# Performance work log

Hardware: AMD Instinct MI355X
Metric: run time of the kernel (lower is better)

Reference implementation:

```python
import jax, jax.numpy as jnp
import numpy as np

HIDDEN = 4096
MOE_INTER = 1024
SHARED_INTER = 4096  # intermediate_size * num_shared_expert
NUM_EXPERTS = 16
TOP_K = 2


def setup_inputs() -> dict:
    key = jax.random.key(0)
    ks = jax.random.split(key, 6)
    s = 0.02
    hidden_states = jax.random.normal(ks[0], (2, 2048, HIDDEN), dtype=jnp.float32)
    gate_w = jax.random.normal(ks[1], (NUM_EXPERTS, HIDDEN), dtype=jnp.float32) * s
    # per-expert SwiGLU weights: gate_up [E, 2I, H], down [E, H, I]
    w_gate_up = jax.random.normal(ks[2], (NUM_EXPERTS, 2 * MOE_INTER, HIDDEN), dtype=jnp.float32) * s
    w_down = jax.random.normal(ks[3], (NUM_EXPERTS, HIDDEN, MOE_INTER), dtype=jnp.float32) * s
    shared_w_gate_up = jax.random.normal(ks[4], (2 * SHARED_INTER, HIDDEN), dtype=jnp.float32) * s
    shared_w_down = jax.random.normal(ks[5], (HIDDEN, SHARED_INTER), dtype=jnp.float32) * s
    return {
        'hidden_states': hidden_states,
        'gate_w': gate_w,
        'w_gate_up': w_gate_up,
        'w_down': w_down,
        'shared_w_gate_up': shared_w_gate_up,
        'shared_w_down': shared_w_down,
    }


def _moe_forward(x, gate_w, w_gate_up, w_down, shared_w_gate_up, shared_w_down):
    orig_shape = x.shape
    x2 = x.reshape(-1, orig_shape[-1])  # [T, H]

    # shared SwiGLU MLP (reduce_results=False in TP; single device here)
    gu_s = x2 @ shared_w_gate_up.T  # [T, 2*Is]
    g_s, u_s = jnp.split(gu_s, 2, axis=-1)
    shared_out = (jax.nn.silu(g_s) * u_s) @ shared_w_down.T  # [T, H]

    # router: softmax -> top-k -> renormalize (top_k > 1)
    logits = x2 @ gate_w.T  # [T, E]
    probs = jax.nn.softmax(logits, axis=-1)
    topk_vals, topk_idx = jax.lax.top_k(probs, TOP_K)  # [T, K]
    topk_vals = topk_vals / jnp.sum(topk_vals, axis=-1, keepdims=True)
    # combine weights [T, E]: sparse top-k weights scattered into dense matrix
    combine = jnp.sum(
        jax.nn.one_hot(topk_idx, NUM_EXPERTS, dtype=x2.dtype) * topk_vals[..., None],
        axis=1,
    )

    # dense per-expert SwiGLU (reference for fused grouped-GEMM)
    gu = jnp.einsum('th,eih->eti', x2, w_gate_up)  # [E, T, 2I]
    g, u = jnp.split(gu, 2, axis=-1)
    act = jax.nn.silu(g) * u  # [E, T, I]
    out_e = jnp.einsum('eti,ehi->eth', act, w_down)  # [E, T, H]
    moe_out = jnp.einsum('eth,te->th', out_e, combine)  # [T, H]

    return (moe_out + shared_out).reshape(orig_shape)


def reference(hidden_states, gate_w, w_gate_up, w_down, shared_w_gate_up, shared_w_down):
    return _moe_forward(hidden_states, gate_w, w_gate_up, w_down,
                        shared_w_gate_up, shared_w_down)
```

## Files before the change

### kernel.cpp

```cpp
#include <hip/hip_runtime.h>
#include <hip/hip_bf16.h>

#define H 4096
#define MOE_I 1024
#define SH_I 4096
#define NE 16
#define T_TOK 4096
#define NPAIR 8192

using bf16x8 = __attribute__((ext_vector_type(8))) short;
using f32x4  = __attribute__((ext_vector_type(4))) float;

__device__ __forceinline__ unsigned short f2bf(float f) {
    unsigned int x = __float_as_uint(f);
    x += 0x7fffu + ((x >> 16) & 1u);
    return (unsigned short)(x >> 16);
}
__device__ __forceinline__ float bf2f(unsigned short u) {
    return __uint_as_float(((unsigned int)u) << 16);
}

__device__ __forceinline__ void gld_lds16(const void* g, void* l) {
    __builtin_amdgcn_global_load_lds(
        (const __attribute__((address_space(1))) void*)g,
        (__attribute__((address_space(3))) void*)l, 16, 0, 0);
}

__global__ __launch_bounds__(256)
void cast_kernel(const float4* __restrict__ src, ushort4* __restrict__ dst, int n4) {
    int i = blockIdx.x * 256 + threadIdx.x;
    if (i < n4) {
        float4 f = src[i];
        ushort4 o;
        o.x = f2bf(f.x); o.y = f2bf(f.y); o.z = f2bf(f.z); o.w = f2bf(f.w);
        dst[i] = o;
    }
}

__global__ __launch_bounds__(256)
void router_kernel(const float* __restrict__ x, const float* __restrict__ gw,
                   int* __restrict__ topk_id, float* __restrict__ topk_w,
                   int* __restrict__ counts) {
    int t = blockIdx.x;
    const float* xr = x + (size_t)t * H;
    __shared__ float lg[NE];
    int tid = threadIdx.x, w = tid >> 6, lane = tid & 63;
#pragma unroll
    for (int i = 0; i < 4; i++) {
        int e = w * 4 + i;
        const float* g = gw + (size_t)e * H;
        float s = 0.f;
        for (int k = lane; k < H; k += 64) s += xr[k] * g[k];
#pragma unroll
        for (int m = 32; m > 0; m >>= 1) s += __shfl_xor(s, m, 64);
        if (lane == 0) lg[e] = s;
    }
    __syncthreads();
    if (tid == 0) {
        int e0 = 0; float l0 = lg[0];
        for (int e = 1; e < NE; e++) if (lg[e] > l0) { l0 = lg[e]; e0 = e; }
        int e1 = -1; float l1 = -1e30f;
        for (int e = 0; e < NE; e++) if (e != e0 && lg[e] > l1) { l1 = lg[e]; e1 = e; }
        float w1 = 1.f / (1.f + __expf(l0 - l1));
        topk_id[2*t] = e0; topk_id[2*t+1] = e1;
        topk_w[2*t] = 1.f - w1; topk_w[2*t+1] = w1;
        atomicAdd(&counts[e0], 1); atomicAdd(&counts[e1], 1);
    }
}

__global__ void scan16(const int* __restrict__ counts, int* __restrict__ offsets,
                       int* __restrict__ cursor) {
    if (threadIdx.x == 0 && blockIdx.x == 0) {
        int s = 0;
        for (int e = 0; e < NE; e++) { offsets[e] = s; cursor[e] = s; s += counts[e]; }
        offsets[NE] = s;
    }
}

__global__ __launch_bounds__(256)
void assign_kernel(const int* __restrict__ topk_id, const float* __restrict__ topk_w,
                   int* __restrict__ cursor, int* __restrict__ perm_tok,
                   float* __restrict__ perm_w) {
    int t = blockIdx.x * blockDim.x + threadIdx.x;
    if (t >= T_TOK) return;
    for (int k = 0; k < 2; k++) {
        int e = topk_id[2*t+k];
        int pos = atomicAdd(&cursor[e], 1);
        perm_tok[pos] = t;
        perm_w[pos] = topk_w[2*t+k];
    }
}

template<int MODE>
__global__ __launch_bounds__(512, 2)
void gemm8(const unsigned short* __restrict__ A0,
           const unsigned short* __restrict__ B0,
           unsigned short* __restrict__ Cb, float* __restrict__ Cf,
           const int* __restrict__ offsets, const int* __restrict__ perm_tok,
           const float* __restrict__ perm_w,
           int K, int N, int M, int ldc) {
    extern __shared__ char smem[];
    int e = 0, off = 0, cnt = M;
    if constexpr (MODE >= 2) { e = blockIdx.z; off = offsets[e]; cnt = offsets[e + 1] - off; }
    const int m0 = blockIdx.y * 256, n0 = blockIdx.x * 256;
    if (m0 >= cnt) return;
    const unsigned short* Bp = B0 + (size_t)e * N * K;

    const int tid = threadIdx.x, w = tid >> 6, lane = tid & 63;
    const int wr = w >> 2, wc = w & 3;
    const int quad = lane >> 4, r16 = lane & 15;

    const unsigned short* srcA[2][2];
    const unsigned short* srcB[2][2];
    int dstA[2][2], dstB[2][2];
#pragma unroll
    for (int kh = 0; kh < 2; kh++)
#pragma unroll
        for (int j = 0; j < 2; j++) {
            int D  = (j * 8 + w) * 1024 + lane * 16;
            int r  = D >> 6;
            int sl = (D >> 4) & 3;
            int sg = sl ^ ((r >> 1) & 3);
            int ra = m0 + r; if (ra > cnt - 1) ra = cnt - 1;
            int rs;
            if constexpr (MODE == 2)      rs = perm_tok[off + ra];
            else if constexpr (MODE == 3) rs = off + ra;
            else                          rs = ra;
            srcA[kh][j] = A0 + (size_t)rs * K + kh * 32 + sg * 8;
            srcB[kh][j] = Bp + (size_t)(n0 + r) * K + kh * 32 + sg * 8;
            dstA[kh][j] = kh * 16384 + (j * 8 + w) * 1024;
            dstB[kh][j] = 32768 + dstA[kh][j];
        }

    const int swz  = (quad ^ ((r16 >> 1) & 3)) * 16;
    const int aoff = (wr * 128 + r16) * 64 + swz;
    const int boff = 32768 + (wc * 64 + r16) * 64 + swz;

    f32x4 acc[8][4];
#pragma unroll
    for (int i = 0; i < 8; i++)
#pragma unroll
        for (int j = 0; j < 4; j++) acc[i][j] = (f32x4){0.f, 0.f, 0.f, 0.f};

    const int nt = K >> 6;

#pragma unroll
    for (int kh = 0; kh < 2; kh++) {
        gld_lds16(srcA[kh][0], smem + dstA[kh][0]);
        gld_lds16(srcA[kh][1], smem + dstA[kh][1]);
        gld_lds16(srcB[kh][0], smem + dstB[kh][0]);
        gld_lds16(srcB[kh][1], smem + dstB[kh][1]);
    }
    {
        int adv0 = (nt > 1) ? 64 : 0;
#pragma unroll
        for (int kh = 0; kh < 2; kh++)
#pragma unroll
            for (int j = 0; j < 2; j++) { srcA[kh][j] += adv0; srcB[kh][j] += adv0; }
    }

    for (int t = 0; t < nt; t++) {
        char* sb = smem + (t & 1) * 65536;
        char* so = smem + ((t + 1) & 1) * 65536;
        const int adv = (t + 2 < nt) ? 64 : 0;
        bf16x8 av[4], bv[4];

        asm volatile("s_waitcnt vmcnt(4)" ::: "memory");
        __builtin_amdgcn_s_barrier();
        asm volatile("" ::: "memory");
        gld_lds16(srcA[0][0], so + dstA[0][0]);
        gld_lds16(srcA[0][1], so + dstA[0][1]);
        srcA[0][0] += adv; srcA[0][1] += adv;
#pragma unroll
        for (int mi = 0; mi < 4; mi++) av[mi] = *(const bf16x8*)(sb + mi * 1024 + aoff);
#pragma unroll
        for (int ni = 0; ni < 4; ni++) bv[ni] = *(const bf16x8*)(sb + ni * 1024 + boff);
        __builtin_amdgcn_s_setprio(1);
#pragma unroll
        for (int mi = 0; mi < 4; mi++)
#pragma unroll
            for (int ni = 0; ni < 4; ni++)
                acc[mi][ni] = __builtin_amdgcn_mfma_f32_16x16x32_bf16(
                    av[mi], bv[ni], acc[mi][ni], 0, 0, 0);
        __builtin_amdgcn_s_setprio(0);
        gld_lds16(srcB[0][0], so + dstB[0][0]);
        gld_lds16(srcB[0][1], so + dstB[0][1]);
        srcB[0][0] += adv; srcB[0][1] += adv;
#pragma unroll
        for (int mi = 0; mi < 4; mi++) av[mi] = *(const bf16x8*)(sb + (mi + 4) * 1024 + aoff);
        __builtin_amdgcn_s_setprio(1);
#pragma unroll
        for (int mi = 0; mi < 4; mi++)
#pragma unroll
            for (int ni = 0; ni < 4; ni++)
                acc[mi + 4][ni] = __builtin_amdgcn_mfma_f32_16x16x32_bf16(
                    av[mi], bv[ni], acc[mi + 4][ni], 0, 0, 0);
        __builtin_amdgcn_s_setprio(0);

        asm volatile("s_waitcnt vmcnt(4)" ::: "memory");
        __builtin_amdgcn_s_barrier();
        asm volatile("" ::: "memory");
        gld_lds16(srcA[1][0], so + dstA[1][0]);
        gld_lds16(srcA[1][1], so + dstA[1][1]);
        srcA[1][0] += adv; srcA[1][1] += adv;
#pragma unroll
        for (int mi = 0; mi < 4; mi++) av[mi] = *(const bf16x8*)(sb + 16384 + mi * 1024 + aoff);
#pragma unroll
        for (int ni = 0; ni < 4; ni++) bv[ni] = *(const bf16x8*)(sb + 16384 + ni * 1024 + boff);
        __builtin_amdgcn_s_setprio(1);
#pragma unroll
        for (int mi = 0; mi < 4; mi++)
#pragma unroll
            for (int ni = 0; ni < 4; ni++)
                acc[mi][ni] = __builtin_amdgcn_mfma_f32_16x16x32_bf16(
                    av[mi], bv[ni], acc[mi][ni], 0, 0, 0);
        __builtin_amdgcn_s_setprio(0);
        gld_lds16(srcB[1][0], so + dstB[1][0]);
        gld_lds16(srcB[1][1], so + dstB[1][1]);
        srcB[1][0] += adv; srcB[1][1] += adv;
#pragma unroll
        for (int mi = 0; mi < 4; mi++) av[mi] = *(const bf16x8*)(sb + 16384 + (mi + 4) * 1024 + aoff);
        __builtin_amdgcn_s_setprio(1);
#pragma unroll
        for (int mi = 0; mi < 4; mi++)
#pragma unroll
            for (int ni = 0; ni < 4; ni++)
                acc[mi + 4][ni] = __builtin_amdgcn_mfma_f32_16x16x32_bf16(
                    av[mi], bv[ni], acc[mi + 4][ni], 0, 0, 0);
        __builtin_amdgcn_s_setprio(0);
    }

    asm volatile("s_waitcnt vmcnt(0)" ::: "memory");

    const int rowlim = cnt - m0;
#pragma unroll
    for (int mi = 0; mi < 8; mi++) {
#pragma unroll
        for (int rr = 0; rr < 4; rr++) {
            int r = wr * 128 + mi * 16 + quad * 4 + rr;
            if (r < rowlim) {
                int tok = 0; float wt = 0.f;
                if constexpr (MODE == 3) {
                    tok = perm_tok[off + m0 + r];
                    wt  = perm_w[off + m0 + r];
                }
#pragma unroll
                for (int ni = 0; ni < 4; ni++) {
                    int col = n0 + wc * 64 + ni * 16 + r16;
                    float v = acc[mi][ni][rr];
                    if constexpr (MODE == 0)
                        Cb[(size_t)(m0 + r) * ldc + col] = f2bf(v);
                    else if constexpr (MODE == 1)
                        Cf[(size_t)(m0 + r) * ldc + col] = v;
                    else if constexpr (MODE == 2)
                        Cb[(size_t)(off + m0 + r) * ldc + col] = f2bf(v);
                    else
                        atomicAdd(&Cf[(size_t)tok * ldc + col], wt * v);
                }
            }
        }
    }
}

template<int SHIFT>
__global__ __launch_bounds__(256)
void swiglu_kernel(const unsigned short* __restrict__ gu, unsigned short* __restrict__ act,
                   long long total) {
    long long idx = ((long long)blockIdx.x * 256 + threadIdx.x) * 8;
    if (idx >= total) return;
    const int half = 1 << SHIFT;
    long long row = idx >> SHIFT;
    int cb = (int)(idx & (half - 1));
    const unsigned short* gp = gu + (row << (SHIFT + 1)) + cb;
    bf16x8 g8 = *(const bf16x8*)gp;
    bf16x8 u8 = *(const bf16x8*)(gp + half);
    bf16x8 res;
#pragma unroll
    for (int i = 0; i < 8; i++) {
        float g = bf2f((unsigned short)g8[i]);
        float u = bf2f((unsigned short)u8[i]);
        float a = g / (1.f + __expf(-g));
        res[i] = (short)f2bf(a * u);
    }
    *(bf16x8*)(act + idx) = res;
}

extern "C" void kernel_launch(void* const* d_in, const int* in_sizes, int n_in,
                              void* d_out, int out_size, void* d_ws, size_t ws_size,
                              hipStream_t stream) {
    const float* x         = (const float*)d_in[0];
    const float* gate_w    = (const float*)d_in[1];
    const float* w_gate_up = (const float*)d_in[2];
    const float* w_down    = (const float*)d_in[3];
    const float* s_wgu     = (const float*)d_in[4];
    const float* s_wd      = (const float*)d_in[5];
    float* out = (float*)d_out;

    char* p = (char*)d_ws;
    auto alloc = [&](size_t bytes) {
        char* q = p;
        p += (bytes + 255) & ~(size_t)255;
        return q;
    };
    unsigned short* x_bf    = (unsigned short*)alloc((size_t)T_TOK * H * 2);
    unsigned short* wgu_bf  = (unsigned short*)alloc((size_t)NE * 2 * MOE_I * H * 2);
    unsigned short* wd_bf   = (unsigned short*)alloc((size_t)NE * H * MOE_I * 2);
    unsigned short* swgu_bf = (unsigned short*)alloc((size_t)2 * SH_I * H * 2);
    unsigned short* swd_bf  = (unsigned short*)alloc((size_t)H * SH_I * 2);
    unsigned short* gu_s    = (unsigned short*)alloc((size_t)T_TOK * 2 * SH_I * 2);
    unsigned short* act_s   = (unsigned short*)alloc((size_t)T_TOK * SH_I * 2);
    unsigned short* gu_e    = (unsigned short*)alloc((size_t)NPAIR * 2 * MOE_I * 2);
    unsigned short* act_e   = (unsigned short*)alloc((size_t)NPAIR * MOE_I * 2);
    int*   topk_id  = (int*)alloc(T_TOK * 2 * 4);
    float* topk_w   = (float*)alloc(T_TOK * 2 * 4);
    int*   counts   = (int*)alloc(NE * 4);
    int*   offsets  = (int*)alloc((NE + 1) * 4);
    int*   cursor   = (int*)alloc(NE * 4);
    int*   perm_tok = (int*)alloc(NPAIR * 4);
    float* perm_w   = (float*)alloc(NPAIR * 4);

    hipMemsetAsync(counts, 0, 768, stream);

    const int SHMEM = 131072;
    static int attr_done = 0;
    if (!attr_done) {
        hipFuncSetAttribute((const void*)gemm8<0>, hipFuncAttributeMaxDynamicSharedMemorySize, SHMEM);
        hipFuncSetAttribute((const void*)gemm8<1>, hipFuncAttributeMaxDynamicSharedMemorySize, SHMEM);
        hipFuncSetAttribute((const void*)gemm8<2>, hipFuncAttributeMaxDynamicSharedMemorySize, SHMEM);
        hipFuncSetAttribute((const void*)gemm8<3>, hipFuncAttributeMaxDynamicSharedMemorySize, SHMEM);
        attr_done = 1;
    }

    auto cast = [&](const float* s, unsigned short* d, size_t n) {
        int n4 = (int)(n / 4);
        cast_kernel<<<(n4 + 255) / 256, 256, 0, stream>>>((const float4*)s, (ushort4*)d, n4);
    };
    cast(x, x_bf, (size_t)T_TOK * H);
    cast(w_gate_up, wgu_bf, (size_t)NE * 2 * MOE_I * H);
    cast(w_down, wd_bf, (size_t)NE * H * MOE_I);
    cast(s_wgu, swgu_bf, (size_t)2 * SH_I * H);
    cast(s_wd, swd_bf, (size_t)H * SH_I);

    router_kernel<<<T_TOK, 256, 0, stream>>>(x, gate_w, topk_id, topk_w, counts);
    scan16<<<1, 64, 0, stream>>>(counts, offsets, cursor);
    assign_kernel<<<16, 256, 0, stream>>>(topk_id, topk_w, cursor, perm_tok, perm_w);

    gemm8<0><<<dim3(2 * SH_I / 256, T_TOK / 256, 1), 512, SHMEM, stream>>>(
        x_bf, swgu_bf, gu_s, nullptr, nullptr, nullptr, nullptr, H, 2 * SH_I, T_TOK, 2 * SH_I);
    swiglu_kernel<12><<<(int)(((long long)T_TOK * SH_I / 8 + 255) / 256), 256, 0, stream>>>(
        gu_s, act_s, (long long)T_TOK * SH_I);
    gemm8<1><<<dim3(H / 256, T_TOK / 256, 1), 512, SHMEM, stream>>>(
        act_s, swd_bf, nullptr, out, nullptr, nullptr, nullptr, SH_I, H, T_TOK, H);

    gemm8<2><<<dim3(2 * MOE_I / 256, T_TOK / 256, NE), 512, SHMEM, stream>>>(
        x_bf, wgu_bf, gu_e, nullptr, offsets, perm_tok, nullptr, H, 2 * MOE_I, 0, 2 * MOE_I);
    swiglu_kernel<10><<<(int)(((long long)NPAIR * MOE_I / 8 + 255) / 256), 256, 0, stream>>>(
        gu_e, act_e, (long long)NPAIR * MOE_I);
    gemm8<3><<<dim3(H / 256, T_TOK / 256, NE), 512, SHMEM, stream>>>(
        act_e, wd_bf, nullptr, out, offsets, perm_tok, perm_w, MOE_I, H, 0, H);
}
```

Measured before the change: 2.073 ms.

## Fuse weight bf16 casting into GEMM B-loads and SwiGLU into gate-up epilogue

The separate fp32-to-bf16 cast kernels for all weight matrices are removed. Each GEMM now reads fp32 weights through registers, converts them with packed bf16 conversion and writes them into swizzled LDS, software-pipelined across the k loop. The gate-up GEMMs interleave gate and up rows so that neighbouring columns pair up, and they apply SiLU*up in the epilogue, which removes the standalone swiglu kernels and the intermediate gate-up buffers. The cost is twice the weight bytes fetched per tile and register-staged loads in place of direct global-to-LDS loads, which may hurt the main-loop throughput.

```diff
diff --git a/kernel.cpp b/kernel.cpp
--- a/kernel.cpp
+++ b/kernel.cpp
@@ -18,6 +18,11 @@
 }
 __device__ __forceinline__ float bf2f(unsigned short u) {
     return __uint_as_float(((unsigned int)u) << 16);
+}
+__device__ __forceinline__ unsigned int cvtpk(float lo, float hi) {
+    unsigned int r;
+    asm("v_cvt_pk_bf16_f32 %0, %1, %2" : "=v"(r) : "v"(lo), "v"(hi));
+    return r;
 }
 
 __device__ __forceinline__ void gld_lds16(const void* g, void* l) {
@@ -94,7 +99,7 @@
 template<int MODE>
 __global__ __launch_bounds__(512, 2)
 void gemm8(const unsigned short* __restrict__ A0,
-           const unsigned short* __restrict__ B0,
+           const float* __restrict__ B0f,
            unsigned short* __restrict__ Cb, float* __restrict__ Cf,
            const int* __restrict__ offsets, const int* __restrict__ perm_tok,
            const float* __restrict__ perm_w,
@@ -104,15 +109,14 @@
     if constexpr (MODE >= 2) { e = blockIdx.z; off = offsets[e]; cnt = offsets[e + 1] - off; }
     const int m0 = blockIdx.y * 256, n0 = blockIdx.x * 256;
     if (m0 >= cnt) return;
-    const unsigned short* Bp = B0 + (size_t)e * N * K;
+    const float* Bp = B0f + (size_t)e * N * K;
 
     const int tid = threadIdx.x, w = tid >> 6, lane = tid & 63;
     const int wr = w >> 2, wc = w & 3;
     const int quad = lane >> 4, r16 = lane & 15;
 
     const unsigned short* srcA[2][2];
-    const unsigned short* srcB[2][2];
-    int dstA[2][2], dstB[2][2];
+    int dstA[2][2];
 #pragma unroll
     for (int kh = 0; kh < 2; kh++)
 #pragma unroll
@@ -127,10 +131,24 @@
             else if constexpr (MODE == 3) rs = off + ra;
             else                          rs = ra;
             srcA[kh][j] = A0 + (size_t)rs * K + kh * 32 + sg * 8;
-            srcB[kh][j] = Bp + (size_t)(n0 + r) * K + kh * 32 + sg * 8;
             dstA[kh][j] = kh * 16384 + (j * 8 + w) * 1024;
-            dstB[kh][j] = 32768 + dstA[kh][j];
-        }
+        }
+
+    const int r_t  = tid >> 4;
+    const int kcol = (tid & 15) * 4;
+    const float* bsrc;
+    size_t rstride;
+    if constexpr (MODE == 0 || MODE == 2) {
+        int n = n0 + r_t;
+        int sr = (n >> 1) + (n & 1) * (N >> 1);
+        bsrc = Bp + (size_t)sr * K + kcol;
+        rstride = (size_t)16 * K;
+    } else {
+        bsrc = Bp + (size_t)(n0 + r_t) * K + kcol;
+        rstride = (size_t)32 * K;
+    }
+    const int bw0 = 32768 + (kcol >> 5) * 16384 + r_t * 64
+                  + ((((kcol & 31) >> 3) ^ ((r_t >> 1) & 3)) * 16) + (kcol & 7) * 2;
 
     const int swz  = (quad ^ ((r16 >> 1) & 3)) * 16;
     const int aoff = (wr * 128 + r16) * 64 + swz;
@@ -144,33 +162,41 @@
 
     const int nt = K >> 6;
 
-#pragma unroll
-    for (int kh = 0; kh < 2; kh++) {
-        gld_lds16(srcA[kh][0], smem + dstA[kh][0]);
-        gld_lds16(srcA[kh][1], smem + dstA[kh][1]);
-        gld_lds16(srcB[kh][0], smem + dstB[kh][0]);
-        gld_lds16(srcB[kh][1], smem + dstB[kh][1]);
+    gld_lds16(srcA[0][0], smem + dstA[0][0]);
+    gld_lds16(srcA[0][1], smem + dstA[0][1]);
+    {
+        float4 b0[8];
+#pragma unroll
+        for (int i = 0; i < 8; i++) b0[i] = *(const float4*)(bsrc + (size_t)i * rstride);
+        gld_lds16(srcA[1][0], smem + dstA[1][0]);
+        gld_lds16(srcA[1][1], smem + dstA[1][1]);
+#pragma unroll
+        for (int i = 0; i < 8; i++) {
+            uint2 u2; u2.x = cvtpk(b0[i].x, b0[i].y); u2.y = cvtpk(b0[i].z, b0[i].w);
+            *(uint2*)(smem + bw0 + i * 2048) = u2;
+        }
     }
     {
         int adv0 = (nt > 1) ? 64 : 0;
 #pragma unroll
         for (int kh = 0; kh < 2; kh++)
 #pragma unroll
-            for (int j = 0; j < 2; j++) { srcA[kh][j] += adv0; srcB[kh][j] += adv0; }
+            for (int j = 0; j < 2; j++) srcA[kh][j] += adv0;
+        bsrc += adv0;
     }
 
     for (int t = 0; t < nt; t++) {
         char* sb = smem + (t & 1) * 65536;
         char* so = smem + ((t + 1) & 1) * 65536;
-        const int adv = (t + 2 < nt) ? 64 : 0;
+        const int advA = (t + 2 < nt) ? 64 : 0;
         bf16x8 av[4], bv[4];
-
-        asm volatile("s_waitcnt vmcnt(4)" ::: "memory");
+        float4 bld[8];
+
+        asm volatile("s_waitcnt lgkmcnt(0)" ::: "memory");
         __builtin_amdgcn_s_barrier();
-        asm volatile("" ::: "memory");
         gld_lds16(srcA[0][0], so + dstA[0][0]);
         gld_lds16(srcA[0][1], so + dstA[0][1]);
-        srcA[0][0] += adv; srcA[0][1] += adv;
+        srcA[0][0] += advA; srcA[0][1] += advA;
 #pragma unroll
         for (int mi = 0; mi < 4; mi++) av[mi] = *(const bf16x8*)(sb + mi * 1024 + aoff);
 #pragma unroll
@@ -183,9 +209,10 @@
                 acc[mi][ni] = __builtin_amdgcn_mfma_f32_16x16x32_bf16(
                     av[mi], bv[ni], acc[mi][ni], 0, 0, 0);
         __builtin_amdgcn_s_setprio(0);
-        gld_lds16(srcB[0][0], so + dstB[0][0]);
-        gld_lds16(srcB[0][1], so + dstB[0][1]);
-        srcB[0][0] += adv; srcB[0][1] += adv;
+        __builtin_amdgcn_sched_barrier(0);
+#pragma unroll
+        for (int i = 0; i < 8; i++) bld[i] = *(const float4*)(bsrc + (size_t)i * rstride);
+        __builtin_amdgcn_sched_barrier(0);
 #pragma unroll
         for (int mi = 0; mi < 4; mi++) av[mi] = *(const bf16x8*)(sb + (mi + 4) * 1024 + aoff);
         __builtin_amdgcn_s_setprio(1);
@@ -197,12 +224,11 @@
                     av[mi], bv[ni], acc[mi + 4][ni], 0, 0, 0);
         __builtin_amdgcn_s_setprio(0);
 
-        asm volatile("s_waitcnt vmcnt(4)" ::: "memory");
+        asm volatile("s_waitcnt vmcnt(10)" ::: "memory");
         __builtin_amdgcn_s_barrier();
-        asm volatile("" ::: "memory");
         gld_lds16(srcA[1][0], so + dstA[1][0]);
         gld_lds16(srcA[1][1], so + dstA[1][1]);
-        srcA[1][0] += adv; srcA[1][1] += adv;
+        srcA[1][0] += advA; srcA[1][1] += advA;
 #pragma unroll
         for (int mi = 0; mi < 4; mi++) av[mi] = *(const bf16x8*)(sb + 16384 + mi * 1024 + aoff);
 #pragma unroll
@@ -215,9 +241,12 @@
                 acc[mi][ni] = __builtin_amdgcn_mfma_f32_16x16x32_bf16(
                     av[mi], bv[ni], acc[mi][ni], 0, 0, 0);
         __builtin_amdgcn_s_setprio(0);
-        gld_lds16(srcB[1][0], so + dstB[1][0]);
-        gld_lds16(srcB[1][1], so + dstB[1][1]);
-        srcB[1][0] += adv; srcB[1][1] += adv;
+#pragma unroll
+        for (int i = 0; i < 8; i++) {
+            uint2 u2; u2.x = cvtpk(bld[i].x, bld[i].y); u2.y = cvtpk(bld[i].z, bld[i].w);
+            *(uint2*)(so + bw0 + i * 2048) = u2;
+        }
+        bsrc += (t + 2 < nt) ? 64 : 0;
 #pragma unroll
         for (int mi = 0; mi < 4; mi++) av[mi] = *(const bf16x8*)(sb + 16384 + (mi + 4) * 1024 + aoff);
         __builtin_amdgcn_s_setprio(1);
@@ -233,56 +262,50 @@
     asm volatile("s_waitcnt vmcnt(0)" ::: "memory");
 
     const int rowlim = cnt - m0;
-#pragma unroll
-    for (int mi = 0; mi < 8; mi++) {
-#pragma unroll
-        for (int rr = 0; rr < 4; rr++) {
-            int r = wr * 128 + mi * 16 + quad * 4 + rr;
-            if (r < rowlim) {
-                int tok = 0; float wt = 0.f;
-                if constexpr (MODE == 3) {
-                    tok = perm_tok[off + m0 + r];
-                    wt  = perm_w[off + m0 + r];
-                }
+    if constexpr (MODE == 0 || MODE == 2) {
+#pragma unroll
+        for (int mi = 0; mi < 8; mi++) {
+#pragma unroll
+            for (int rr = 0; rr < 4; rr++) {
+                int r = wr * 128 + mi * 16 + quad * 4 + rr;
 #pragma unroll
                 for (int ni = 0; ni < 4; ni++) {
-                    int col = n0 + wc * 64 + ni * 16 + r16;
-                    float v = acc[mi][ni][rr];
-                    if constexpr (MODE == 0)
-                        Cb[(size_t)(m0 + r) * ldc + col] = f2bf(v);
-                    else if constexpr (MODE == 1)
-                        Cf[(size_t)(m0 + r) * ldc + col] = v;
-                    else if constexpr (MODE == 2)
-                        Cb[(size_t)(off + m0 + r) * ldc + col] = f2bf(v);
-                    else
-                        atomicAdd(&Cf[(size_t)tok * ldc + col], wt * v);
+                    float g = acc[mi][ni][rr];
+                    float u = __shfl_xor(g, 1, 64);
+                    if (((r16 & 1) == 0) && (r < rowlim)) {
+                        float a = (g / (1.f + __expf(-g))) * u;
+                        size_t row = (MODE == 0) ? (size_t)(m0 + r) : (size_t)(off + m0 + r);
+                        int colh = (n0 >> 1) + wc * 32 + ni * 8 + (r16 >> 1);
+                        Cb[row * ldc + colh] = f2bf(a);
+                    }
                 }
             }
         }
-    }
-}
-
-template<int SHIFT>
-__global__ __launch_bounds__(256)
-void swiglu_kernel(const unsigned short* __restrict__ gu, unsigned short* __restrict__ act,
-                   long long total) {
-    long long idx = ((long long)blockIdx.x * 256 + threadIdx.x) * 8;
-    if (idx >= total) return;
-    const int half = 1 << SHIFT;
-    long long row = idx >> SHIFT;
-    int cb = (int)(idx & (half - 1));
-    const unsigned short* gp = gu + (row << (SHIFT + 1)) + cb;
-    bf16x8 g8 = *(const bf16x8*)gp;
-    bf16x8 u8 = *(const bf16x8*)(gp + half);
-    bf16x8 res;
-#pragma unroll
-    for (int i = 0; i < 8; i++) {
-        float g = bf2f((unsigned short)g8[i]);
-        float u = bf2f((unsigned short)u8[i]);
-        float a = g / (1.f + __expf(-g));
-        res[i] = (short)f2bf(a * u);
-    }
-    *(bf16x8*)(act + idx) = res;
+    } else {
+#pragma unroll
+        for (int mi = 0; mi < 8; mi++) {
+#pragma unroll
+            for (int rr = 0; rr < 4; rr++) {
+                int r = wr * 128 + mi * 16 + quad * 4 + rr;
+                if (r < rowlim) {
+                    int tok = 0; float wt = 0.f;
+                    if constexpr (MODE == 3) {
+                        tok = perm_tok[off + m0 + r];
+                        wt  = perm_w[off + m0 + r];
+                    }
+#pragma unroll
+                    for (int ni = 0; ni < 4; ni++) {
+                        int col = n0 + wc * 64 + ni * 16 + r16;
+                        float v = acc[mi][ni][rr];
+                        if constexpr (MODE == 1)
+                            Cf[(size_t)(m0 + r) * ldc + col] = v;
+                        else
+                            atomicAdd(&Cf[(size_t)tok * ldc + col], wt * v);
+                    }
+                }
+            }
+        }
+    }
 }
 
 extern "C" void kernel_launch(void* const* d_in, const int* in_sizes, int n_in,
@@ -302,15 +325,9 @@
         p += (bytes + 255) & ~(size_t)255;
         return q;
     };
-    unsigned short* x_bf    = (unsigned short*)alloc((size_t)T_TOK * H * 2);
-    unsigned short* wgu_bf  = (unsigned short*)alloc((size_t)NE * 2 * MOE_I * H * 2);
-    unsigned short* wd_bf   = (unsigned short*)alloc((size_t)NE * H * MOE_I * 2);
-    unsigned short* swgu_bf = (unsigned short*)alloc((size_t)2 * SH_I * H * 2);
-    unsigned short* swd_bf  = (unsigned short*)alloc((size_t)H * SH_I * 2);
-    unsigned short* gu_s    = (unsigned short*)alloc((size_t)T_TOK * 2 * SH_I * 2);
-    unsigned short* act_s   = (unsigned short*)alloc((size_t)T_TOK * SH_I * 2);
-    unsigned short* gu_e    = (unsigned short*)alloc((size_t)NPAIR * 2 * MOE_I * 2);
-    unsigned short* act_e   = (unsigned short*)alloc((size_t)NPAIR * MOE_I * 2);
+    unsigned short* x_bf   = (unsigned short*)alloc((size_t)T_TOK * H * 2);
+    unsigned short* act_s  = (unsigned short*)alloc((size_t)T_TOK * SH_I * 2);
+    unsigned short* act_e  = (unsigned short*)alloc((size_t)NPAIR * MOE_I * 2);
     int*   topk_id  = (int*)alloc(T_TOK * 2 * 4);
     float* topk_w   = (float*)alloc(T_TOK * 2 * 4);
     int*   counts   = (int*)alloc(NE * 4);
@@ -331,31 +348,22 @@
         attr_done = 1;
     }
 
-    auto cast = [&](const float* s, unsigned short* d, size_t n) {
-        int n4 = (int)(n / 4);
-        cast_kernel<<<(n4 + 255) / 256, 256, 0, stream>>>((const float4*)s, (ushort4*)d, n4);
-    };
-    cast(x, x_bf, (size_t)T_TOK * H);
-    cast(w_gate_up, wgu_bf, (size_t)NE * 2 * MOE_I * H);
-    cast(w_down, wd_bf, (size_t)NE * H * MOE_I);
-    cast(s_wgu, swgu_bf, (size_t)2 * SH_I * H);
-    cast(s_wd, swd_bf, (size_t)H * SH_I);
+    {
+        int n4 = (int)((size_t)T_TOK * H / 4);
+        cast_kernel<<<(n4 + 255) / 256, 256, 0, stream>>>((const float4*)x, (ushort4*)x_bf, n4);
+    }
 
     router_kernel<<<T_TOK, 256, 0, stream>>>(x, gate_w, topk_id, topk_w, counts);
     scan16<<<1, 64, 0, stream>>>(counts, offsets, cursor);
     assign_kernel<<<16, 256, 0, stream>>>(topk_id, topk_w, cursor, perm_tok, perm_w);
 
     gemm8<0><<<dim3(2 * SH_I / 256, T_TOK / 256, 1), 512, SHMEM, stream>>>(
-        x_bf, swgu_bf, gu_s, nullptr, nullptr, nullptr, nullptr, H, 2 * SH_I, T_TOK, 2 * SH_I);
-    swiglu_kernel<12><<<(int)(((long long)T_TOK * SH_I / 8 + 255) / 256), 256, 0, stream>>>(
-        gu_s, act_s, (long long)T_TOK * SH_I);
+        x_bf, s_wgu, act_s, nullptr, nullptr, nullptr, nullptr, H, 2 * SH_I, T_TOK, SH_I);
     gemm8<1><<<dim3(H / 256, T_TOK / 256, 1), 512, SHMEM, stream>>>(
-        act_s, swd_bf, nullptr, out, nullptr, nullptr, nullptr, SH_I, H, T_TOK, H);
+        act_s, s_wd, nullptr, out, nullptr, nullptr, nullptr, SH_I, H, T_TOK, H);
 
     gemm8<2><<<dim3(2 * MOE_I / 256, T_TOK / 256, NE), 512, SHMEM, stream>>>(
-        x_bf, wgu_bf, gu_e, nullptr, offsets, perm_tok, nullptr, H, 2 * MOE_I, 0, 2 * MOE_I);
-    swiglu_kernel<10><<<(int)(((long long)NPAIR * MOE_I / 8 + 255) / 256), 256, 0, stream>>>(
-        gu_e, act_e, (long long)NPAIR * MOE_I);
+        x_bf, w_gate_up, act_e, nullptr, offsets, perm_tok, nullptr, H, 2 * MOE_I, 0, MOE_I);
     gemm8<3><<<dim3(H / 256, T_TOK / 256, NE), 512, SHMEM, stream>>>(
-        act_e, wd_bf, nullptr, out, offsets, perm_tok, perm_w, MOE_I, H, 0, H);
-}
+        act_e, w_down, nullptr, out, offsets, perm_tok, perm_w, MOE_I, H, 0, H);
+}
```

Measured after the change: 2.079 ms. About the same (+0.3%).
